# Kernel optimization log

Measured on AMD Instinct MI355X. Metric: run time of the kernel, lower is better.

## Reference

```python
import jax, jax.numpy as jnp
import numpy as np
from jax import lax

B, T, I, H, O = 64, 2048, 128, 256, 1


def setup_inputs() -> dict:
    key = jax.random.key(0)
    ks = jax.random.split(key, 8)
    lim_ih = 1.0 / np.sqrt(H)
    inp = {
        "xd": jax.random.normal(ks[0], (B, T, I), jnp.float32),
        "w": jax.random.normal(ks[1], (B, T, I), jnp.float32),
        # eqx.nn.LSTMCell params: gates stacked [i, f, g, o] along first axis
        "W_ih": jax.random.uniform(ks[2], (4 * H, I), jnp.float32, -lim_ih, lim_ih),
        "b_ih": jax.random.uniform(ks[3], (4 * H,), jnp.float32, -lim_ih, lim_ih),
        "W_hh": jax.random.uniform(ks[4], (4 * H, H), jnp.float32, -lim_ih, lim_ih),
        "b_hh": jax.random.uniform(ks[5], (4 * H,), jnp.float32, -lim_ih, lim_ih),
        "W_out": jax.random.uniform(ks[6], (O, H), jnp.float32, -lim_ih, lim_ih),
        "b_out": jax.random.uniform(ks[7], (O,), jnp.float32, -lim_ih, lim_ih),
    }
    return inp


def reference(xd, w, W_ih, b_ih, W_hh, b_hh, W_out, b_out):
    # Input gating (elementwise), then precompute the input-to-gates GEMM for
    # the whole sequence (mathematically identical to doing it per step).
    gated = xd * jax.nn.sigmoid(w)                       # [B,T,I]
    x_part = jnp.einsum("bti,gi->btg", gated, W_ih) + b_ih  # [B,T,4H]
    x_part = jnp.swapaxes(x_part, 0, 1)                  # [T,B,4H] for scan

    def step(state, xp):
        h, c = state
        z = xp + h @ W_hh.T + b_hh                       # [B,4H]
        i, f, g, o = jnp.split(z, 4, axis=-1)            # eqx gate order i,f,g,o
        c = jax.nn.sigmoid(f) * c + jax.nn.sigmoid(i) * jnp.tanh(g)
        h = jax.nn.sigmoid(o) * jnp.tanh(c)
        return (h, c), None

    init = (jnp.zeros((B, H), xd.dtype), jnp.zeros((B, H), xd.dtype))
    (h_T, _), _ = lax.scan(step, init, x_part)
    return h_T @ W_out.T + b_out                         # [B,O]
```

## Files before the change

kernel.cpp:

```cpp
#include <hip/hip_runtime.h>
#include <hip/hip_fp16.h>
#include <stdint.h>


#define NB 64
#define NT 2048
#define NI 128
#define NH 256

typedef _Float16 h8_t __attribute__((ext_vector_type(8)));
typedef _Float16 h4_t __attribute__((ext_vector_type(4)));
typedef float f4_t __attribute__((ext_vector_type(4)));

__device__ __forceinline__ float sigm(float x) {
  return __builtin_amdgcn_rcpf(1.f + __expf(-x));
}
__device__ __forceinline__ float tanh_f(float x) {
  return 1.f - 2.f * __builtin_amdgcn_rcpf(1.f + __expf(2.f * x));
}


__launch_bounds__(256, 1)
__global__ void lstm_persist(
    const float* __restrict__ xd, const float* __restrict__ w,
    const float* __restrict__ W_ih, const float* __restrict__ b_ih,
    const float* __restrict__ W_hh, const float* __restrict__ b_hh,
    const float* __restrict__ W_out, const float* __restrict__ b_out,
    float* __restrict__ out, uint64_t* ex)
{
  const int bid = blockIdx.x;
  const int g = bid & 7;
  const int p = bid >> 3;
  const int tid = threadIdx.x;
  const int lane = tid & 63;
  const int wv = tid >> 6;

  __shared__ _Float16 Alds[16][392];
  __shared__ float Zlds[128][17];

  for (int i = tid; i < 16 * 392; i += 256) (&Alds[0][0])[i] = (_Float16)0.f;

  const int q  = lane >> 4;
  const int cc = lane & 15;

  h8_t wf[2][12];
  for (int nt = 0; nt < 2; ++nt) {
    int r = 16 * (2 * wv + nt) + cc;
    int R = (r & 3) * NH + p * 32 + (r >> 2);
    for (int kt = 0; kt < 12; ++kt) {
      int k = kt * 32 + q * 8;
      const float* s = (k < NI) ? (W_ih + (size_t)R * NI + k)
                                : (W_hh + (size_t)R * NH + (k - NI));
      f4_t lo = *(const f4_t*)s;
      f4_t hi = *(const f4_t*)(s + 4);
      h8_t hh;
      hh[0] = (_Float16)lo[0]; hh[1] = (_Float16)lo[1];
      hh[2] = (_Float16)lo[2]; hh[3] = (_Float16)lo[3];
      hh[4] = (_Float16)hi[0]; hh[5] = (_Float16)hi[1];
      hh[6] = (_Float16)hi[2]; hh[7] = (_Float16)hi[3];
      wf[nt][kt] = hh;
    }
  }

  const int bl = tid >> 5;
  const int jj = tid & 31;
  float bias[4];
  #pragma unroll
  for (int gate = 0; gate < 4; ++gate)
    bias[gate] = b_ih[gate * NH + p * 32 + jj] + b_hh[gate * NH + p * 32 + jj];

  int pidx[7];
  #pragma unroll
  for (int s7 = 0; s7 < 7; ++s7) {
    int ps = (s7 < p) ? s7 : s7 + 1;
    pidx[s7] = g * 2048 + ps * 256 + bl * 32 + jj;
  }
  uint64_t* const myslot0 = ex + g * 2048 + p * 256 + bl * 32 + jj;

  float creg = 0.f;
  float hreg = 0.f;
  const size_t xbase = ((size_t)(g * 8 + bl) * NT) * NI + jj * 4;

  __syncthreads();

  for (int t = 0; t < NT; ++t) {
    f4_t xv = *(const f4_t*)(xd + xbase + (size_t)t * NI);
    f4_t wg = *(const f4_t*)(w  + xbase + (size_t)t * NI);

    if (t > 0) {
      const uint64_t* base = ex + (t & 1) * 16384;
      unsigned need = 0x7f;
      uint64_t v[7];
      while (need) {
        #pragma unroll
        for (int s7 = 0; s7 < 7; ++s7)
          if (need & (1u << s7))
            v[s7] = __hip_atomic_load(base + pidx[s7], __ATOMIC_RELAXED,
                                      __HIP_MEMORY_SCOPE_AGENT);
        #pragma unroll
        for (int s7 = 0; s7 < 7; ++s7)
          if ((need & (1u << s7)) && (unsigned)(v[s7] >> 32) == (unsigned)t) {
            int ps = (s7 < p) ? s7 : s7 + 1;
            Alds[bl][NI + ps * 32 + jj] =
                (_Float16)__uint_as_float((unsigned)v[s7]);
            need &= ~(1u << s7);
          }
      }
    }

    h4_t gx;
    gx[0] = (_Float16)(xv[0] * sigm(wg[0]));
    gx[1] = (_Float16)(xv[1] * sigm(wg[1]));
    gx[2] = (_Float16)(xv[2] * sigm(wg[2]));
    gx[3] = (_Float16)(xv[3] * sigm(wg[3]));
    *(h4_t*)(&Alds[bl][jj * 4]) = gx;
    __syncthreads();

    f4_t acc0 = {0.f, 0.f, 0.f, 0.f}, acc1 = {0.f, 0.f, 0.f, 0.f};
    #pragma unroll
    for (int kt = 0; kt < 12; ++kt) {
      h8_t af = *(const h8_t*)(&Alds[cc][kt * 32 + q * 8]);
      acc0 = __builtin_amdgcn_mfma_f32_16x16x32_f16(af, wf[0][kt], acc0, 0, 0, 0);
      acc1 = __builtin_amdgcn_mfma_f32_16x16x32_f16(af, wf[1][kt], acc1, 0, 0, 0);
    }
    if (q < 2) {
      #pragma unroll
      for (int r = 0; r < 4; ++r) {
        Zlds[16 * (2 * wv)     + cc][q * 4 + r] = acc0[r];
        Zlds[16 * (2 * wv + 1) + cc][q * 4 + r] = acc1[r];
      }
    }
    __syncthreads();

    float zi = Zlds[jj * 4 + 0][bl] + bias[0];
    float zf = Zlds[jj * 4 + 1][bl] + bias[1];
    float zg = Zlds[jj * 4 + 2][bl] + bias[2];
    float zo = Zlds[jj * 4 + 3][bl] + bias[3];
    creg = sigm(zf) * creg + sigm(zi) * tanh_f(zg);
    hreg = sigm(zo) * tanh_f(creg);
    Alds[bl][NI + p * 32 + jj] = (_Float16)hreg;
    uint64_t pay = ((uint64_t)(unsigned)(t + 1) << 32) | __float_as_uint(hreg);
    __hip_atomic_store(myslot0 + ((t + 1) & 1) * 16384, pay,
                       __ATOMIC_RELAXED, __HIP_MEMORY_SCOPE_AGENT);
  }

  if (p == 0) {
    float sum = hreg * W_out[jj];
    unsigned need = 0x7f;
    uint64_t v[7];
    float hv[7];
    while (need) {
      #pragma unroll
      for (int s7 = 0; s7 < 7; ++s7)
        if (need & (1u << s7))
          v[s7] = __hip_atomic_load(ex + pidx[s7], __ATOMIC_RELAXED,
                                    __HIP_MEMORY_SCOPE_AGENT);
      #pragma unroll
      for (int s7 = 0; s7 < 7; ++s7)
        if ((need & (1u << s7)) && (unsigned)(v[s7] >> 32) == (unsigned)NT) {
          hv[s7] = __uint_as_float((unsigned)v[s7]);
          need &= ~(1u << s7);
        }
    }
    #pragma unroll
    for (int s7 = 0; s7 < 7; ++s7) {
      int ps = (s7 < p) ? s7 : s7 + 1;
      sum += hv[s7] * W_out[ps * 32 + jj];
    }
    #pragma unroll
    for (int m = 16; m >= 1; m >>= 1) sum += __shfl_xor(sum, m, 64);
    if (jj == 0) out[g * 8 + bl] = sum + b_out[0];
  }
}

extern "C" void kernel_launch(void* const* d_in, const int* in_sizes, int n_in,
                              void* d_out, int out_size, void* d_ws, size_t ws_size,
                              hipStream_t stream) {
  (void)in_sizes; (void)n_in; (void)out_size; (void)ws_size;
  const float* xd    = (const float*)d_in[0];
  const float* w     = (const float*)d_in[1];
  const float* W_ih  = (const float*)d_in[2];
  const float* b_ih  = (const float*)d_in[3];
  const float* W_hh  = (const float*)d_in[4];
  const float* b_hh  = (const float*)d_in[5];
  const float* W_out = (const float*)d_in[6];
  const float* b_out = (const float*)d_in[7];
  uint64_t* ex = (uint64_t*)d_ws;
  lstm_persist<<<dim3(64), dim3(256), 0, stream>>>(
      xd, w, W_ih, b_ih, W_hh, b_hh, W_out, b_out, (float*)d_out, ex);
}
```

Measured before the change: 4.362 ms.

## Use raw sc0 global loads for cross-block exchange with runtime coherence probe

Replaces agent-scope atomic loads and stores in the per-step hidden-state exchange with inline-asm global loads (sc0) and plain stores, issuing all seven loads before one waitcnt. A startup handshake probes whether these weaker accesses stay visible across blocks and falls back to the atomic path if not. The loop is also unrolled by two, with x/w loads prefetched two steps ahead. This aims to cut the latency of the spin-wait on each recurrent step, but adds probe overhead and relies on cache-coherence behaviour that is not guaranteed.

After: 4.952 ms. 13.5% more time.

```diff
diff --git a/kernel.cpp b/kernel.cpp
--- a/kernel.cpp
+++ b/kernel.cpp
@@ -8,6 +8,10 @@
 #define NI 128
 #define NH 256
 
+#define PROBE_TAG 0x7E570001u
+#define PRE_TAG   0x5EED0001u
+#define VERD_TAG  0x5EED0002u
+
 typedef _Float16 h8_t __attribute__((ext_vector_type(8)));
 typedef _Float16 h4_t __attribute__((ext_vector_type(4)));
 typedef float f4_t __attribute__((ext_vector_type(4)));
@@ -19,6 +23,122 @@
   return 1.f - 2.f * __builtin_amdgcn_rcpf(1.f + __expf(2.f * x));
 }
 
+__device__ __forceinline__ void fast_sweep7(const uint64_t* fb, const int* po,
+                                            uint64_t* v) {
+  asm volatile(
+      "global_load_dwordx2 %0, %7, %14 sc0\n\t"
+      "global_load_dwordx2 %1, %8, %14 sc0\n\t"
+      "global_load_dwordx2 %2, %9, %14 sc0\n\t"
+      "global_load_dwordx2 %3, %10, %14 sc0\n\t"
+      "global_load_dwordx2 %4, %11, %14 sc0\n\t"
+      "global_load_dwordx2 %5, %12, %14 sc0\n\t"
+      "global_load_dwordx2 %6, %13, %14 sc0\n\t"
+      "s_waitcnt vmcnt(0)"
+      : "=&v"(v[0]), "=&v"(v[1]), "=&v"(v[2]), "=&v"(v[3]), "=&v"(v[4]),
+        "=&v"(v[5]), "=&v"(v[6])
+      : "v"(po[0]), "v"(po[1]), "v"(po[2]), "v"(po[3]), "v"(po[4]),
+        "v"(po[5]), "v"(po[6]), "s"(fb)
+      : "memory");
+}
+
+__device__ __forceinline__ void fast_store(uint64_t* fb, int boff,
+                                           uint64_t pay) {
+  asm volatile("global_store_dwordx2 %0, %1, %2"
+               :: "v"(boff), "v"(pay), "s"(fb)
+               : "memory");
+}
+
+
+#define STEP(T, XV, WGV) do {                                               \
+  const int tt = (T);                                                       \
+  if (tt > 0) {                                                             \
+    unsigned need = 0x7f;                                                   \
+    if (fastmode) {                                                         \
+      const uint64_t* fb = exf + ((tt & 1) << 14);                          \
+      while (need) {                                                        \
+        uint64_t v[7];                                                      \
+        fast_sweep7(fb, poff, v);                                           \
+        _Pragma("unroll")                                                   \
+        for (int s7 = 0; s7 < 7; ++s7)                                      \
+          if ((need & (1u << s7)) &&                                        \
+              (unsigned)(v[s7] >> 32) == (unsigned)tt) {                    \
+            int ps = (s7 < p) ? s7 : s7 + 1;                                \
+            Alds[bl][NI + ps * 32 + jj] =                                   \
+                (_Float16)__uint_as_float((unsigned)v[s7]);                 \
+            need &= ~(1u << s7);                                            \
+          }                                                                 \
+      }                                                                     \
+    } else {                                                                \
+      const uint64_t* base = exs + ((tt & 1) << 14);                        \
+      uint64_t v[7];                                                        \
+      while (need) {                                                        \
+        _Pragma("unroll")                                                   \
+        for (int s7 = 0; s7 < 7; ++s7)                                      \
+          if (need & (1u << s7))                                            \
+            v[s7] = __hip_atomic_load(base + pidx[s7], __ATOMIC_RELAXED,    \
+                                      __HIP_MEMORY_SCOPE_AGENT);            \
+        _Pragma("unroll")                                                   \
+        for (int s7 = 0; s7 < 7; ++s7)                                      \
+          if ((need & (1u << s7)) &&                                        \
+              (unsigned)(v[s7] >> 32) == (unsigned)tt) {                    \
+            int ps = (s7 < p) ? s7 : s7 + 1;                                \
+            Alds[bl][NI + ps * 32 + jj] =                                   \
+                (_Float16)__uint_as_float((unsigned)v[s7]);                 \
+            need &= ~(1u << s7);                                            \
+          }                                                                 \
+      }                                                                     \
+    }                                                                       \
+  }                                                                         \
+  {                                                                         \
+    h4_t gx;                                                                \
+    gx[0] = (_Float16)(XV[0] * sigm(WGV[0]));                               \
+    gx[1] = (_Float16)(XV[1] * sigm(WGV[1]));                               \
+    gx[2] = (_Float16)(XV[2] * sigm(WGV[2]));                               \
+    gx[3] = (_Float16)(XV[3] * sigm(WGV[3]));                               \
+    *(h4_t*)(&Alds[bl][jj * 4]) = gx;                                       \
+  }                                                                         \
+  if (tt + 2 < NT) {   \
+    XV  = *(const f4_t*)(xd + xbase + (size_t)(tt + 2) * NI);               \
+    WGV = *(const f4_t*)(w  + xbase + (size_t)(tt + 2) * NI);               \
+  }                                                                         \
+  __syncthreads();                          \
+  {                                                                         \
+    f4_t acc0 = {0.f, 0.f, 0.f, 0.f}, acc1 = {0.f, 0.f, 0.f, 0.f};         \
+    _Pragma("unroll")                                                       \
+    for (int kt = 0; kt < 12; ++kt) {                                       \
+      h8_t af = *(const h8_t*)(&Alds[cc][kt * 32 + q * 8]);                 \
+      acc0 = __builtin_amdgcn_mfma_f32_16x16x32_f16(af, wf[0][kt], acc0,    \
+                                                    0, 0, 0);               \
+      acc1 = __builtin_amdgcn_mfma_f32_16x16x32_f16(af, wf[1][kt], acc1,    \
+                                                    0, 0, 0);               \
+    }                                                                       \
+    if (q < 2) {                                                            \
+      _Pragma("unroll")                                                     \
+      for (int r = 0; r < 4; ++r) {                                         \
+        Zlds[16 * (2 * wv)     + cc][q * 4 + r] = acc0[r];                  \
+        Zlds[16 * (2 * wv + 1) + cc][q * 4 + r] = acc1[r];                  \
+      }                                                                     \
+    }                                                                       \
+  }                                                                         \
+  __syncthreads();                               \
+  {                                                                         \
+    float zi = Zlds[jj * 4 + 0][bl] + bias[0];                              \
+    float zf = Zlds[jj * 4 + 1][bl] + bias[1];                              \
+    float zg = Zlds[jj * 4 + 2][bl] + bias[2];                              \
+    float zo = Zlds[jj * 4 + 3][bl] + bias[3];                              \
+    creg = sigm(zf) * creg + sigm(zi) * tanh_f(zg);                         \
+    hreg = sigm(zo) * tanh_f(creg);                                         \
+    uint64_t pay =                                                          \
+        ((uint64_t)(unsigned)(tt + 1) << 32) | __float_as_uint(hreg);       \
+    if (fastmode) {                                                         \
+      fast_store(exf + (((tt + 1) & 1) << 14), myoff, pay);                 \
+    } else {                                                                \
+      __hip_atomic_store(exs + (((tt + 1) & 1) << 14) + myidx, pay,         \
+                         __ATOMIC_RELAXED, __HIP_MEMORY_SCOPE_AGENT);       \
+    }                                                                       \
+    Alds[bl][NI + p * 32 + jj] = (_Float16)hreg;     \
+  }                                                                         \
+} while (0)
 
 __launch_bounds__(256, 1)
 __global__ void lstm_persist(
@@ -26,7 +146,7 @@
     const float* __restrict__ W_ih, const float* __restrict__ b_ih,
     const float* __restrict__ W_hh, const float* __restrict__ b_hh,
     const float* __restrict__ W_out, const float* __restrict__ b_out,
-    float* __restrict__ out, uint64_t* ex)
+    float* __restrict__ out, uint64_t* ex, int mode)
 {
   const int bid = blockIdx.x;
   const int g = bid & 7;
@@ -37,6 +157,7 @@
 
   __shared__ _Float16 Alds[16][392];
   __shared__ float Zlds[128][17];
+  __shared__ int fastmode_sh;
 
   for (int i = tid; i < 16 * 392; i += 256) (&Alds[0][0])[i] = (_Float16)0.f;
 
@@ -69,98 +190,118 @@
   for (int gate = 0; gate < 4; ++gate)
     bias[gate] = b_ih[gate * NH + p * 32 + jj] + b_hh[gate * NH + p * 32 + jj];
 
-  int pidx[7];
+  int pidx[7], poff[7];
   #pragma unroll
   for (int s7 = 0; s7 < 7; ++s7) {
     int ps = (s7 < p) ? s7 : s7 + 1;
     pidx[s7] = g * 2048 + ps * 256 + bl * 32 + jj;
-  }
-  uint64_t* const myslot0 = ex + g * 2048 + p * 256 + bl * 32 + jj;
+    poff[s7] = pidx[s7] * 8;
+  }
+  const int myidx = g * 2048 + p * 256 + bl * 32 + jj;
+  const int myoff = myidx * 8;
+
+  uint64_t* const exf = ex;
+  uint64_t* const exs = mode ? (ex + 32768) : ex;
+  uint64_t* const exv = ex + 65536;
+
+  int fastmode = 0;
+  if (mode) {
+    {
+      uint64_t pv[7];
+      fast_sweep7(exf, poff, pv);
+      asm volatile("" :: "v"(pv[0]));
+    }
+    __syncthreads();
+    if (tid == 0)
+      __hip_atomic_store(exv + bid, ((uint64_t)PRE_TAG << 32) | 1u,
+                         __ATOMIC_RELAXED, __HIP_MEMORY_SCOPE_AGENT);
+    if (tid < 8) {
+      uint64_t vv;
+      do {
+        vv = __hip_atomic_load(exv + 8 * tid + g, __ATOMIC_RELAXED,
+                               __HIP_MEMORY_SCOPE_AGENT);
+        unsigned tg = (unsigned)(vv >> 32);
+        if (tg == PRE_TAG || tg == VERD_TAG) break;
+      } while (1);
+    }
+    __syncthreads();
+    fast_store(exf, myoff, ((uint64_t)PROBE_TAG << 32) | (unsigned)bid);
+    unsigned need = 0x7f;
+    for (int sw = 0; sw < 3000 && need; ++sw) {
+      uint64_t v[7];
+      fast_sweep7(exf, poff, v);
+      #pragma unroll
+      for (int s7 = 0; s7 < 7; ++s7)
+        if ((need & (1u << s7)) && (unsigned)(v[s7] >> 32) == PROBE_TAG)
+          need &= ~(1u << s7);
+    }
+    int allok = __syncthreads_and(need == 0);
+    if (tid == 0)
+      __hip_atomic_store(exv + bid,
+                         ((uint64_t)VERD_TAG << 32) | (unsigned)(allok ? 1 : 0),
+                         __ATOMIC_RELAXED, __HIP_MEMORY_SCOPE_AGENT);
+    if (tid == 0) {
+      int fm = 1;
+      for (int m8 = 0; m8 < 8; ++m8) {
+        uint64_t vv;
+        do {
+          vv = __hip_atomic_load(exv + 8 * m8 + g, __ATOMIC_RELAXED,
+                                 __HIP_MEMORY_SCOPE_AGENT);
+        } while ((unsigned)(vv >> 32) != VERD_TAG);
+        fm &= (int)((unsigned)vv & 1u);
+      }
+      fastmode_sh = fm;
+    }
+    __syncthreads();
+    fastmode = fastmode_sh;
+  }
 
   float creg = 0.f;
   float hreg = 0.f;
   const size_t xbase = ((size_t)(g * 8 + bl) * NT) * NI + jj * 4;
 
+  f4_t xvA = *(const f4_t*)(xd + xbase);
+  f4_t wgA = *(const f4_t*)(w  + xbase);
+  f4_t xvB = *(const f4_t*)(xd + xbase + NI);
+  f4_t wgB = *(const f4_t*)(w  + xbase + NI);
+
   __syncthreads();
 
-  for (int t = 0; t < NT; ++t) {
-    f4_t xv = *(const f4_t*)(xd + xbase + (size_t)t * NI);
-    f4_t wg = *(const f4_t*)(w  + xbase + (size_t)t * NI);
-
-    if (t > 0) {
-      const uint64_t* base = ex + (t & 1) * 16384;
-      unsigned need = 0x7f;
+  for (int t = 0; t < NT; t += 2) {
+    STEP(t,     xvA, wgA);
+    STEP(t + 1, xvB, wgB);
+  }
+
+  if (p == 0) {
+    float sum = hreg * W_out[jj];
+    unsigned need = 0x7f;
+    float hv[7];
+    if (fastmode) {
+      while (need) {
+        uint64_t v[7];
+        fast_sweep7(exf, poff, v);
+        #pragma unroll
+        for (int s7 = 0; s7 < 7; ++s7)
+          if ((need & (1u << s7)) && (unsigned)(v[s7] >> 32) == (unsigned)NT) {
+            hv[s7] = __uint_as_float((unsigned)v[s7]);
+            need &= ~(1u << s7);
+          }
+      }
+    } else {
       uint64_t v[7];
       while (need) {
         #pragma unroll
         for (int s7 = 0; s7 < 7; ++s7)
           if (need & (1u << s7))
-            v[s7] = __hip_atomic_load(base + pidx[s7], __ATOMIC_RELAXED,
+            v[s7] = __hip_atomic_load(exs + pidx[s7], __ATOMIC_RELAXED,
                                       __HIP_MEMORY_SCOPE_AGENT);
         #pragma unroll
         for (int s7 = 0; s7 < 7; ++s7)
-          if ((need & (1u << s7)) && (unsigned)(v[s7] >> 32) == (unsigned)t) {
-            int ps = (s7 < p) ? s7 : s7 + 1;
-            Alds[bl][NI + ps * 32 + jj] =
-                (_Float16)__uint_as_float((unsigned)v[s7]);
+          if ((need & (1u << s7)) && (unsigned)(v[s7] >> 32) == (unsigned)NT) {
+            hv[s7] = __uint_as_float((unsigned)v[s7]);
             need &= ~(1u << s7);
           }
       }
-    }
-
-    h4_t gx;
-    gx[0] = (_Float16)(xv[0] * sigm(wg[0]));
-    gx[1] = (_Float16)(xv[1] * sigm(wg[1]));
-    gx[2] = (_Float16)(xv[2] * sigm(wg[2]));
-    gx[3] = (_Float16)(xv[3] * sigm(wg[3]));
-    *(h4_t*)(&Alds[bl][jj * 4]) = gx;
-    __syncthreads();
-
-    f4_t acc0 = {0.f, 0.f, 0.f, 0.f}, acc1 = {0.f, 0.f, 0.f, 0.f};
-    #pragma unroll
-    for (int kt = 0; kt < 12; ++kt) {
-      h8_t af = *(const h8_t*)(&Alds[cc][kt * 32 + q * 8]);
-      acc0 = __builtin_amdgcn_mfma_f32_16x16x32_f16(af, wf[0][kt], acc0, 0, 0, 0);
-      acc1 = __builtin_amdgcn_mfma_f32_16x16x32_f16(af, wf[1][kt], acc1, 0, 0, 0);
-    }
-    if (q < 2) {
-      #pragma unroll
-      for (int r = 0; r < 4; ++r) {
-        Zlds[16 * (2 * wv)     + cc][q * 4 + r] = acc0[r];
-        Zlds[16 * (2 * wv + 1) + cc][q * 4 + r] = acc1[r];
-      }
-    }
-    __syncthreads();
-
-    float zi = Zlds[jj * 4 + 0][bl] + bias[0];
-    float zf = Zlds[jj * 4 + 1][bl] + bias[1];
-    float zg = Zlds[jj * 4 + 2][bl] + bias[2];
-    float zo = Zlds[jj * 4 + 3][bl] + bias[3];
-    creg = sigm(zf) * creg + sigm(zi) * tanh_f(zg);
-    hreg = sigm(zo) * tanh_f(creg);
-    Alds[bl][NI + p * 32 + jj] = (_Float16)hreg;
-    uint64_t pay = ((uint64_t)(unsigned)(t + 1) << 32) | __float_as_uint(hreg);
-    __hip_atomic_store(myslot0 + ((t + 1) & 1) * 16384, pay,
-                       __ATOMIC_RELAXED, __HIP_MEMORY_SCOPE_AGENT);
-  }
-
-  if (p == 0) {
-    float sum = hreg * W_out[jj];
-    unsigned need = 0x7f;
-    uint64_t v[7];
-    float hv[7];
-    while (need) {
-      #pragma unroll
-      for (int s7 = 0; s7 < 7; ++s7)
-        if (need & (1u << s7))
-          v[s7] = __hip_atomic_load(ex + pidx[s7], __ATOMIC_RELAXED,
-                                    __HIP_MEMORY_SCOPE_AGENT);
-      #pragma unroll
-      for (int s7 = 0; s7 < 7; ++s7)
-        if ((need & (1u << s7)) && (unsigned)(v[s7] >> 32) == (unsigned)NT) {
-          hv[s7] = __uint_as_float((unsigned)v[s7]);
-          need &= ~(1u << s7);
-        }
     }
     #pragma unroll
     for (int s7 = 0; s7 < 7; ++s7) {
@@ -176,7 +317,7 @@
 extern "C" void kernel_launch(void* const* d_in, const int* in_sizes, int n_in,
                               void* d_out, int out_size, void* d_ws, size_t ws_size,
                               hipStream_t stream) {
-  (void)in_sizes; (void)n_in; (void)out_size; (void)ws_size;
+  (void)in_sizes; (void)n_in; (void)out_size;
   const float* xd    = (const float*)d_in[0];
   const float* w     = (const float*)d_in[1];
   const float* W_ih  = (const float*)d_in[2];
@@ -186,6 +327,8 @@
   const float* W_out = (const float*)d_in[6];
   const float* b_out = (const float*)d_in[7];
   uint64_t* ex = (uint64_t*)d_ws;
+  const size_t NEEDED = (size_t)65600 * 8;
+  int mode = (ws_size >= NEEDED) ? 1 : 0;
   lstm_persist<<<dim3(64), dim3(256), 0, stream>>>(
-      xd, w, W_ih, b_ih, W_hh, b_hh, W_out, b_out, (float*)d_out, ex);
-}
+      xd, w, W_ih, b_ih, W_hh, b_hh, W_out, b_out, (float*)d_out, ex, mode);
+}
```
